# Kernel optimization log

Hardware: AMD Instinct MI355X
Metric: run time of the kernel (lower is better)

## Reference

```python
import jax, jax.numpy as jnp
import numpy as np

N = 100_000      # nodes
E = 1_600_000    # edges
IN = 256         # inchannel
H, D = 8, 16     # num_heads, out_feats per head (outchannel = 128)
SLOPE = 0.2      # DGL GATv2Conv default negative_slope


def setup_inputs() -> dict:
    key = jax.random.key(0)
    ks = jax.random.split(key, 8)
    s = 1.0 / np.sqrt(IN)
    return {
        "x": jax.random.normal(ks[0], (N, IN), jnp.float32),
        "src": jax.random.randint(ks[1], (E,), 0, N, jnp.int32),
        "dst": jax.random.randint(ks[2], (E,), 0, N, jnp.int32),
        "W_src": jax.random.uniform(ks[3], (IN, H * D), jnp.float32, -s, s),
        "b_src": jnp.zeros((H * D,), jnp.float32),
        "W_dst": jax.random.uniform(ks[4], (IN, H * D), jnp.float32, -s, s),
        "b_dst": jnp.zeros((H * D,), jnp.float32),
        "attn": jax.random.normal(ks[5], (H, D), jnp.float32) * 0.1,
        "W_res": jax.random.uniform(ks[6], (IN, H * D), jnp.float32, -s, s),
        "b_res": jnp.zeros((H * D,), jnp.float32),
    }


def reference(x, src, dst, W_src, b_src, W_dst, b_dst, attn, W_res, b_res):
    # GATv2: separate src/dst projections (share_weights=False)
    el = (x @ W_src + b_src).reshape(N, H, D)   # feat_src, (N,H,D)
    er = (x @ W_dst + b_dst).reshape(N, H, D)   # feat_dst, (N,H,D)

    # per-edge: e = LeakyReLU(el[u] + er[v]); score = sum(e * attn, -1)
    e = el[src] + er[dst]                        # (E,H,D)
    e = jnp.where(e > 0, e, SLOPE * e)           # LeakyReLU(0.2)
    score = jnp.einsum('ehd,hd->eh', e, attn)    # (E,H)

    # edge softmax over incoming edges of each destination node
    m = jax.ops.segment_max(score, dst, num_segments=N)   # (N,H)
    a = jnp.exp(score - m[dst])
    denom = jax.ops.segment_sum(a, dst, num_segments=N)   # (N,H)
    alpha = a / denom[dst]                                 # (E,H)

    # weighted aggregation of source features
    rst = jax.ops.segment_sum(alpha[:, :, None] * el[src], dst, num_segments=N)  # (N,H,D)

    # residual (in_feats != H*D -> linear res_fc)
    res = (x @ W_res + b_res).reshape(N, H, D)
    return (rst + res).reshape(N, H * D)
```

## Files before the change

kernel.cpp:

```cpp
#include <hip/hip_runtime.h>
#include <hip/hip_bf16.h>
#include <cstdint>

#define SLOPE 0.2f
#define IN_F 256
#define HD 128
#define BSH 8
#define BMAX 8192

typedef __attribute__((ext_vector_type(8))) short bf16x8;
typedef __attribute__((ext_vector_type(4))) float f32x4;

union BF8 { bf16x8 v; __hip_bfloat16 h[8]; };

__device__ inline float bf_lo(unsigned u) { unsigned w = u << 16; return __builtin_bit_cast(float, w); }
__device__ inline float bf_hi(unsigned u) { unsigned w = u & 0xffff0000u; return __builtin_bit_cast(float, w); }

__global__ void detect_kernel(const unsigned int* __restrict__ xw,
                              int* __restrict__ flag) {
    __shared__ int sh[256];
    int t = threadIdx.x;
    int cnt = 0;
    for (int i = t; i < 4096; i += 256) {
        unsigned e = (xw[i] >> 7) & 0xFF;
        cnt += (e >= 64u && e <= 191u) ? 1 : 0;
    }
    sh[t] = cnt;
    __syncthreads();
    for (int s = 128; s > 0; s >>= 1) {
        if (t < s) sh[t] += sh[t + s];
        __syncthreads();
    }
    if (t == 0) flag[0] = (sh[0] > 3300) ? 1 : 0;
}

__global__ void prep_kernel(const void* __restrict__ Ws, const void* __restrict__ Wd,
                            const void* __restrict__ Wr,
                            const void* __restrict__ bs, const void* __restrict__ bd,
                            const void* __restrict__ br,
                            const void* __restrict__ attn,
                            const int* __restrict__ flag,
                            __hip_bfloat16* __restrict__ Wp,
                            float* __restrict__ bfv, float* __restrict__ af) {
    int t = blockIdx.x * blockDim.x + threadIdx.x;
    int isb = flag[0];
    if (t < 3 * 8 * 8 * 64) {
        int lane = t & 63;
        int nt = (t >> 6) & 7;
        int kt = (t >> 9) & 7;
        int m  = t >> 12;
        const void* W = (m == 0) ? Ws : (m == 1) ? Wd : Wr;
        int n = nt * 16 + (lane & 15);
        int k0 = kt * 32 + (lane >> 4) * 8;
        size_t off = ((((size_t)m * 8 + kt) * 8 + nt) * 64 + lane) * 8;
#pragma unroll
        for (int j = 0; j < 8; j++) {
            size_t gi = (size_t)(k0 + j) * HD + n;
            Wp[off + j] = isb ? ((const __hip_bfloat16*)W)[gi]
                              : __float2bfloat16(((const float*)W)[gi]);
        }
    } else if (t < 3 * 8 * 8 * 64 + 384) {
        int j = t - 3 * 8 * 8 * 64;
        const void* b = (j < 128) ? bs : (j < 256 ? bd : br);
        int i = j & 127;
        bfv[j] = isb ? __bfloat162float(((const __hip_bfloat16*)b)[i])
                     : ((const float*)b)[i];
    } else if (t < 3 * 8 * 8 * 64 + 384 + 128) {
        int j = t - 3 * 8 * 8 * 64 - 384;
        af[j] = isb ? __bfloat162float(((const __hip_bfloat16*)attn)[j])
                    : ((const float*)attn)[j];
    }
}

template <bool ISB>
__device__ __forceinline__ void proj_body(
    const void* __restrict__ xv, const __hip_bfloat16* __restrict__ Wp,
    const float* __restrict__ bfv,
    __hip_bfloat16* __restrict__ el, __hip_bfloat16* __restrict__ er,
    __hip_bfloat16* __restrict__ resm,
    __hip_bfloat16* __restrict__ sbuf, int Nn) {
    int wv = threadIdx.x >> 6;
    int lane = threadIdx.x & 63;
    int r_base = blockIdx.x * 128 + wv * 32;

    BF8 a[2][8];
#pragma unroll
    for (int j = 0; j < 2; j++) {
        int row = r_base + j * 16 + (lane & 15);
        if (row >= Nn) row = Nn - 1;
        size_t xo = (size_t)row * IN_F + (lane >> 4) * 8;
#pragma unroll
        for (int kt = 0; kt < 8; kt++) {
            if (ISB) {
                a[j][kt].v = *(const bf16x8*)((const __hip_bfloat16*)xv + xo + kt * 32);
            } else {
                float4 p0 = *(const float4*)((const float*)xv + xo + kt * 32);
                float4 p1 = *(const float4*)((const float*)xv + xo + kt * 32 + 4);
                a[j][kt].h[0] = __float2bfloat16(p0.x); a[j][kt].h[1] = __float2bfloat16(p0.y);
                a[j][kt].h[2] = __float2bfloat16(p0.z); a[j][kt].h[3] = __float2bfloat16(p0.w);
                a[j][kt].h[4] = __float2bfloat16(p1.x); a[j][kt].h[5] = __float2bfloat16(p1.y);
                a[j][kt].h[6] = __float2bfloat16(p1.z); a[j][kt].h[7] = __float2bfloat16(p1.w);
            }
        }
    }

    int col = lane & 15;
    int quad = lane >> 4;

    for (int m = 0; m < 3; m++) {
        f32x4 acc[2][8];
#pragma unroll
        for (int j = 0; j < 2; j++)
#pragma unroll
            for (int nt = 0; nt < 8; nt++) acc[j][nt] = (f32x4){0.f, 0.f, 0.f, 0.f};

        for (int h = 0; h < 2; h++) {
            __syncthreads();
#pragma unroll
            for (int i = 0; i < 8; i++) {
                int chunk = i * 256 + threadIdx.x;
                *(bf16x8*)(sbuf + (size_t)chunk * 8) =
                    *(const bf16x8*)(Wp + (size_t)m * 32768 + (size_t)h * 16384 + (size_t)chunk * 8);
            }
            __syncthreads();
#pragma unroll
            for (int k4 = 0; k4 < 4; k4++) {
#pragma unroll
                for (int nt = 0; nt < 8; nt++) {
                    bf16x8 b = *(const bf16x8*)(sbuf + ((size_t)(k4 * 8 + nt)) * 512 + (size_t)lane * 8);
                    acc[0][nt] = __builtin_amdgcn_mfma_f32_16x16x32_bf16(a[0][h * 4 + k4].v, b, acc[0][nt], 0, 0, 0);
                    acc[1][nt] = __builtin_amdgcn_mfma_f32_16x16x32_bf16(a[1][h * 4 + k4].v, b, acc[1][nt], 0, 0, 0);
                }
            }
        }

        __hip_bfloat16* outp = (m == 0) ? el : (m == 1) ? er : resm;
#pragma unroll
        for (int j = 0; j < 2; j++) {
#pragma unroll
            for (int nt = 0; nt < 8; nt++) {
                float bv = bfv[m * HD + nt * 16 + col];
#pragma unroll
                for (int r = 0; r < 4; r++) {
                    int row = r_base + j * 16 + quad * 4 + r;
                    if (row < Nn)
                        outp[(size_t)row * HD + nt * 16 + col] = __float2bfloat16(acc[j][nt][r] + bv);
                }
            }
        }
    }
}

__global__ __launch_bounds__(256) void proj_mfma_kernel(
    const void* __restrict__ xv, const __hip_bfloat16* __restrict__ Wp,
    const float* __restrict__ bfv, const int* __restrict__ flag,
    __hip_bfloat16* __restrict__ el, __hip_bfloat16* __restrict__ er,
    __hip_bfloat16* __restrict__ resm, int Nn) {
    __shared__ __hip_bfloat16 sbuf[16384];
    if (flag[0]) proj_body<true>(xv, Wp, bfv, el, er, resm, sbuf, Nn);
    else         proj_body<false>(xv, Wp, bfv, el, er, resm, sbuf, Nn);
}

__global__ __launch_bounds__(256) void bhist_kernel(
    const int* __restrict__ dst, int* __restrict__ bcnt, int E, int NB) {
    __shared__ int cnt[512];
    int t = threadIdx.x;
    cnt[t] = 0; cnt[t + 256] = 0;
    __syncthreads();
    for (int i = blockIdx.x * 256 + t; i < E; i += gridDim.x * 256)
        atomicAdd(&cnt[dst[i] >> BSH], 1);
    __syncthreads();
    for (int j = t; j < NB; j += 256) {
        int c = cnt[j];
        if (c) atomicAdd(&bcnt[j], c);
    }
}

__global__ __launch_bounds__(512) void bscan_kernel(
    const int* __restrict__ bcnt, int* __restrict__ bbase,
    int* __restrict__ bcur, int NB) {
    __shared__ int sh[512];
    int t = threadIdx.x;
    sh[t] = (t < NB) ? bcnt[t] : 0;
    __syncthreads();
    for (int off = 1; off < 512; off <<= 1) {
        int x = sh[t];
        int y = (t >= off) ? sh[t - off] : 0;
        __syncthreads();
        sh[t] = x + y;
        __syncthreads();
    }
    if (t < NB) {
        int e = (t == 0) ? 0 : sh[t - 1];
        bbase[t] = e;
        bcur[t * 16] = e;
    }
}

__global__ void bin_kernel(const int* __restrict__ src, const int* __restrict__ dst,
                           int* __restrict__ bcur, unsigned* __restrict__ pairs, int E) {
    int t = blockIdx.x * blockDim.x + threadIdx.x;
    if (t < E) {
        int d = dst[t];
        int s = src[t];
        int b = d >> BSH;
        int pos = atomicAdd(&bcur[b * 16], 1);
        pairs[pos] = ((unsigned)(d & ((1 << BSH) - 1)) << 17) | (unsigned)s;
    }
}

__global__ __launch_bounds__(256) void scatter2_kernel(
    const unsigned* __restrict__ pairs, const int* __restrict__ bbase,
    const int* __restrict__ bcnt,
    int* __restrict__ deg, int* __restrict__ basep,
    int* __restrict__ srcs_sorted, int Nn) {
    __shared__ unsigned sp[BMAX];
    __shared__ int cnt[256];
    __shared__ int cur[256];
    int b = blockIdx.x;
    int t = threadIdx.x;
    int e0 = bbase[b];
    int ec = bcnt[b];
    bool fit = (ec <= BMAX);
    cnt[t] = 0;
    __syncthreads();
    for (int i = t; i < ec; i += 256) {
        unsigned p = pairs[e0 + i];
        if (fit) sp[i] = p;
        atomicAdd(&cnt[p >> 17], 1);
    }
    __syncthreads();
    int c = cnt[t];
    cur[t] = c;
    __syncthreads();
    for (int off = 1; off < 256; off <<= 1) {
        int x = cur[t];
        int y = (t >= off) ? cur[t - off] : 0;
        __syncthreads();
        cur[t] = x + y;
        __syncthreads();
    }
    int excl = cur[t] - c;
    int v = (b << BSH) + t;
    if (v < Nn) {
        deg[v] = c;
        basep[v] = e0 + excl;
    }
    __syncthreads();
    cur[t] = excl;
    __syncthreads();
    for (int i = t; i < ec; i += 256) {
        unsigned p = fit ? sp[i] : pairs[e0 + i];
        int hi = p >> 17;
        int lpos = atomicAdd(&cur[hi], 1);
        srcs_sorted[e0 + lpos] = (int)(p & 0x1FFFFu);
    }
}

__device__ __forceinline__ void agg_edge(unsigned u, float er0, float er1,
                                         float a0, float a1,
                                         float& l, float& acc0, float& acc1) {
    float x0 = bf_lo(u), x1 = bf_hi(u);
    float t0 = x0 + er0, t1 = x1 + er1;
    t0 = fmaxf(t0, SLOPE * t0); t1 = fmaxf(t1, SLOPE * t1);
    float p = t0 * a0 + t1 * a1;
    p += __shfl_xor(p, 1); p += __shfl_xor(p, 2); p += __shfl_xor(p, 4);
    float w = __expf(p);
    l += w; acc0 += w * x0; acc1 += w * x1;
}

__global__ __launch_bounds__(256) void node_agg_kernel(
    const unsigned* __restrict__ el32,
    const unsigned* __restrict__ er32,
    const unsigned* __restrict__ res32,
    const float* __restrict__ af,
    const int* __restrict__ base,
    const int* __restrict__ deg,
    const int* __restrict__ srcs_sorted,
    const int* __restrict__ flag,
    void* __restrict__ out,
    int Nn) {
    int wv = threadIdx.x >> 6;
    int lane = threadIdx.x & 63;
    int v = blockIdx.x * 4 + wv;
    if (v >= Nn) return;

    unsigned uer = er32[(size_t)v * 64 + lane];
    float er0 = bf_lo(uer), er1 = bf_hi(uer);
    float a0 = af[2 * lane], a1 = af[2 * lane + 1];
    int b0 = base[v];
    int dv = deg[v];

    float l = 0.f, acc0 = 0.f, acc1 = 0.f;
    for (int i0 = 0; i0 < dv; i0 += 64) {
        int chunk = dv - i0; if (chunk > 64) chunk = 64;
        int idx = (lane < chunk) ? srcs_sorted[b0 + i0 + lane] : 0;
        int i = 0;
        for (; i + 3 < chunk; i += 4) {
            int s0 = __shfl(idx, i);
            int s1 = __shfl(idx, i + 1);
            int s2 = __shfl(idx, i + 2);
            int s3 = __shfl(idx, i + 3);
            unsigned u0 = el32[(size_t)s0 * 64 + lane];
            unsigned u1 = el32[(size_t)s1 * 64 + lane];
            unsigned u2 = el32[(size_t)s2 * 64 + lane];
            unsigned u3 = el32[(size_t)s3 * 64 + lane];
            agg_edge(u0, er0, er1, a0, a1, l, acc0, acc1);
            agg_edge(u1, er0, er1, a0, a1, l, acc0, acc1);
            agg_edge(u2, er0, er1, a0, a1, l, acc0, acc1);
            agg_edge(u3, er0, er1, a0, a1, l, acc0, acc1);
        }
        for (; i < chunk; i++) {
            int s0 = __shfl(idx, i);
            unsigned u0 = el32[(size_t)s0 * 64 + lane];
            agg_edge(u0, er0, er1, a0, a1, l, acc0, acc1);
        }
    }

    float inv = (dv > 0 && l > 0.f) ? (1.f / l) : 0.f;
    unsigned ur = res32[(size_t)v * 64 + lane];
    float o0 = acc0 * inv + bf_lo(ur);
    float o1 = acc1 * inv + bf_hi(ur);
    if (flag[0]) {
        __hip_bfloat16 h0 = __float2bfloat16(o0);
        __hip_bfloat16 h1 = __float2bfloat16(o1);
        unsigned pk = (unsigned)__builtin_bit_cast(unsigned short, h0)
                    | ((unsigned)__builtin_bit_cast(unsigned short, h1) << 16);
        ((unsigned*)out)[(size_t)v * 64 + lane] = pk;
    } else {
        ((float2*)out)[(size_t)v * 64 + lane] = make_float2(o0, o1);
    }
}

extern "C" void kernel_launch(void* const* d_in, const int* in_sizes, int n_in,
                              void* d_out, int out_size, void* d_ws, size_t ws_size,
                              hipStream_t stream) {
    const void* x    = d_in[0];
    const int*  src  = (const int*)d_in[1];
    const int*  dst  = (const int*)d_in[2];
    const void* Ws   = d_in[3];
    const void* bs   = d_in[4];
    const void* Wd   = d_in[5];
    const void* bd   = d_in[6];
    const void* attn = d_in[7];
    const void* Wr   = d_in[8];
    const void* br   = d_in[9];

    const int Nn = in_sizes[0] / IN_F;
    const int E  = in_sizes[1];
    const int NB = (Nn + (1 << BSH) - 1) >> BSH;

    char* w = (char*)d_ws;
    auto take = [&](size_t bytes) {
        char* p = w;
        w += (bytes + 255) & ~(size_t)255;
        return p;
    };
    int*   flag = (int*)take(256);
    __hip_bfloat16* Wp = (__hip_bfloat16*)take((size_t)3 * 8 * 8 * 64 * 8 * 2);
    float* bfv  = (float*)take((size_t)384 * 4);
    float* af   = (float*)take((size_t)128 * 4);
    __hip_bfloat16* el   = (__hip_bfloat16*)take((size_t)Nn * HD * 2);
    __hip_bfloat16* er   = (__hip_bfloat16*)take((size_t)Nn * HD * 2);
    __hip_bfloat16* resm = (__hip_bfloat16*)take((size_t)Nn * HD * 2);
    int* deg     = (int*)take((size_t)Nn * 4);
    int* base    = (int*)take((size_t)Nn * 4);
    int* bcnt    = (int*)take((size_t)NB * 4);
    int* bbase   = (int*)take((size_t)NB * 4);
    int* bcur    = (int*)take((size_t)NB * 16 * 4);
    unsigned* pairs  = (unsigned*)take((size_t)E * 4);
    int* srcs_sorted = (int*)take((size_t)E * 4);

    hipMemsetAsync(bcnt, 0, (size_t)NB * 4, stream);

    detect_kernel<<<1, 256, 0, stream>>>((const unsigned int*)x, flag);

    prep_kernel<<<(3 * 8 * 8 * 64 + 512 + 255) / 256, 256, 0, stream>>>(
        Ws, Wd, Wr, bs, bd, br, attn, flag, Wp, bfv, af);

    proj_mfma_kernel<<<(Nn + 127) / 128, 256, 0, stream>>>(
        x, Wp, bfv, flag, el, er, resm, Nn);

    bhist_kernel<<<640, 256, 0, stream>>>(dst, bcnt, E, NB);
    bscan_kernel<<<1, 512, 0, stream>>>(bcnt, bbase, bcur, NB);
    bin_kernel<<<(E + 255) / 256, 256, 0, stream>>>(src, dst, bcur, pairs, E);
    scatter2_kernel<<<NB, 256, 0, stream>>>(pairs, bbase, bcnt, deg, base, srcs_sorted, Nn);

    node_agg_kernel<<<(Nn + 3) / 4, 256, 0, stream>>>(
        (const unsigned*)el, (const unsigned*)er, (const unsigned*)resm,
        af, base, deg, srcs_sorted, flag, d_out, Nn);
}
```

Before: 449.9 us.

## Double-buffer weight tiles in LDS with async global-to-LDS loads in projection

The projection kernel now keeps two 32 KB LDS buffers and prefetches the next weight slab while MFMAs consume the current one, cutting the synchronization points per slab from two to one. When available, it uses the global_load_lds builtin so weights go straight from global memory to LDS without passing through registers. LDS use doubles to 64 KB per block and the launch bounds ask for 2 blocks per CU, which may limit occupancy or force register spills. The direct-to-LDS path issues no explicit vmcnt wait before the barrier, which could be a correctness risk.

After: 448.4 us. No clear change (-0.3%).

```diff
diff --git a/kernel.cpp b/kernel.cpp
--- a/kernel.cpp
+++ b/kernel.cpp
@@ -15,6 +15,16 @@
 
 __device__ inline float bf_lo(unsigned u) { unsigned w = u << 16; return __builtin_bit_cast(float, w); }
 __device__ inline float bf_hi(unsigned u) { unsigned w = u & 0xffff0000u; return __builtin_bit_cast(float, w); }
+
+__device__ __forceinline__ void stage16(const void* g, void* l) {
+#if __has_builtin(__builtin_amdgcn_global_load_lds)
+    __builtin_amdgcn_global_load_lds(
+        (const __attribute__((address_space(1))) void*)g,
+        (__attribute__((address_space(3))) void*)l, 16, 0, 0);
+#else
+    *(bf16x8*)l = *(const bf16x8*)g;
+#endif
+}
 
 __global__ void detect_kernel(const unsigned int* __restrict__ xw,
                               int* __restrict__ flag) {
@@ -79,8 +89,9 @@
     __hip_bfloat16* __restrict__ el, __hip_bfloat16* __restrict__ er,
     __hip_bfloat16* __restrict__ resm,
     __hip_bfloat16* __restrict__ sbuf, int Nn) {
-    int wv = threadIdx.x >> 6;
-    int lane = threadIdx.x & 63;
+    int tid = threadIdx.x;
+    int wv = tid >> 6;
+    int lane = tid & 63;
     int r_base = blockIdx.x * 128 + wv * 32;
 
     BF8 a[2][8];
@@ -107,56 +118,74 @@
     int col = lane & 15;
     int quad = lane >> 4;
 
-    for (int m = 0; m < 3; m++) {
-        f32x4 acc[2][8];
-#pragma unroll
-        for (int j = 0; j < 2; j++)
-#pragma unroll
-            for (int nt = 0; nt < 8; nt++) acc[j][nt] = (f32x4){0.f, 0.f, 0.f, 0.f};
-
-        for (int h = 0; h < 2; h++) {
-            __syncthreads();
+#pragma unroll
+    for (int i = 0; i < 8; i++) {
+        int c = i * 256 + tid;
+        stage16(Wp + (size_t)c * 8, sbuf + (size_t)c * 8);
+    }
+    __syncthreads();
+
+    f32x4 acc[2][8];
+
+#pragma unroll
+    for (int s = 0; s < 6; s++) {
+        const int m = s >> 1, h = s & 1;
+
+        if (s < 5) {
+            __hip_bfloat16* db = sbuf + (size_t)((s + 1) & 1) * 16384;
+            const __hip_bfloat16* sb = Wp + (size_t)(s + 1) * 16384;
 #pragma unroll
             for (int i = 0; i < 8; i++) {
-                int chunk = i * 256 + threadIdx.x;
-                *(bf16x8*)(sbuf + (size_t)chunk * 8) =
-                    *(const bf16x8*)(Wp + (size_t)m * 32768 + (size_t)h * 16384 + (size_t)chunk * 8);
+                int c = i * 256 + tid;
+                stage16(sb + (size_t)c * 8, db + (size_t)c * 8);
             }
-            __syncthreads();
-#pragma unroll
-            for (int k4 = 0; k4 < 4; k4++) {
+        }
+
+        if (h == 0) {
+#pragma unroll
+            for (int j = 0; j < 2; j++)
+#pragma unroll
+                for (int nt = 0; nt < 8; nt++) acc[j][nt] = (f32x4){0.f, 0.f, 0.f, 0.f};
+        }
+
+        const __hip_bfloat16* rb = sbuf + (size_t)(s & 1) * 16384;
+#pragma unroll
+        for (int k4 = 0; k4 < 4; k4++) {
+#pragma unroll
+            for (int nt = 0; nt < 8; nt++) {
+                bf16x8 b = *(const bf16x8*)(rb + ((size_t)(k4 * 8 + nt)) * 512 + (size_t)lane * 8);
+                acc[0][nt] = __builtin_amdgcn_mfma_f32_16x16x32_bf16(a[0][h * 4 + k4].v, b, acc[0][nt], 0, 0, 0);
+                acc[1][nt] = __builtin_amdgcn_mfma_f32_16x16x32_bf16(a[1][h * 4 + k4].v, b, acc[1][nt], 0, 0, 0);
+            }
+        }
+
+        __syncthreads();
+
+        if (h == 1) {
+            __hip_bfloat16* outp = (m == 0) ? el : (m == 1) ? er : resm;
+#pragma unroll
+            for (int j = 0; j < 2; j++) {
 #pragma unroll
                 for (int nt = 0; nt < 8; nt++) {
-                    bf16x8 b = *(const bf16x8*)(sbuf + ((size_t)(k4 * 8 + nt)) * 512 + (size_t)lane * 8);
-                    acc[0][nt] = __builtin_amdgcn_mfma_f32_16x16x32_bf16(a[0][h * 4 + k4].v, b, acc[0][nt], 0, 0, 0);
-                    acc[1][nt] = __builtin_amdgcn_mfma_f32_16x16x32_bf16(a[1][h * 4 + k4].v, b, acc[1][nt], 0, 0, 0);
+                    float bv = bfv[m * HD + nt * 16 + col];
+#pragma unroll
+                    for (int r = 0; r < 4; r++) {
+                        int row = r_base + j * 16 + quad * 4 + r;
+                        if (row < Nn)
+                            outp[(size_t)row * HD + nt * 16 + col] = __float2bfloat16(acc[j][nt][r] + bv);
+                    }
                 }
             }
         }
-
-        __hip_bfloat16* outp = (m == 0) ? el : (m == 1) ? er : resm;
-#pragma unroll
-        for (int j = 0; j < 2; j++) {
-#pragma unroll
-            for (int nt = 0; nt < 8; nt++) {
-                float bv = bfv[m * HD + nt * 16 + col];
-#pragma unroll
-                for (int r = 0; r < 4; r++) {
-                    int row = r_base + j * 16 + quad * 4 + r;
-                    if (row < Nn)
-                        outp[(size_t)row * HD + nt * 16 + col] = __float2bfloat16(acc[j][nt][r] + bv);
-                }
-            }
-        }
-    }
-}
-
-__global__ __launch_bounds__(256) void proj_mfma_kernel(
+    }
+}
+
+__global__ __launch_bounds__(256, 2) void proj_mfma_kernel(
     const void* __restrict__ xv, const __hip_bfloat16* __restrict__ Wp,
     const float* __restrict__ bfv, const int* __restrict__ flag,
     __hip_bfloat16* __restrict__ el, __hip_bfloat16* __restrict__ er,
     __hip_bfloat16* __restrict__ resm, int Nn) {
-    __shared__ __hip_bfloat16 sbuf[16384];
+    __shared__ __hip_bfloat16 sbuf[32768];
     if (flag[0]) proj_body<true>(xv, Wp, bfv, el, er, resm, sbuf, Nn);
     else         proj_body<false>(xv, Wp, bfv, el, er, resm, sbuf, Nn);
 }
```
